# Kernel optimization log

Measured on AMD Instinct MI355X. Metric: run time of the kernel, lower is better.

Reference implementation:

```python
import jax, jax.numpy as jnp
import numpy as np
from jax import lax

PC_RANGE = (-54.0, -54.0, -5.0, 54.0, 54.0, 3.0)
HEIGHTS = (-1.0, 0.0, 1.0)  # all within [z_min, z_max]
IMG_H, IMG_W = 256.0, 704.0  # batch_input_shape of the camera image
BN_EPS = 1e-5


def setup_inputs() -> dict:
    key = jax.random.key(0)
    ks = jax.random.split(key, 11)
    d = {}
    d['radar_bev'] = jax.random.normal(ks[0], (2, 384, 180, 180), jnp.float32)
    d['img_feat'] = jax.random.normal(ks[1], (2, 256, 64, 176), jnp.float32)
    d['lidar2img'] = jax.random.normal(ks[2], (2, 3, 4), jnp.float32)
    d['w1'] = jax.random.normal(ks[3], (384, 256, 1, 1), jnp.float32) * 0.05
    d['bn1'] = jax.random.uniform(ks[4], (4, 384), jnp.float32, 0.1, 1.0)
    d['w2'] = jax.random.normal(ks[5], (384, 384, 3, 3), jnp.float32) * 0.02
    d['bn2'] = jax.random.uniform(ks[6], (4, 384), jnp.float32, 0.1, 1.0)
    d['wf1'] = jax.random.normal(ks[7], (384, 768, 3, 3), jnp.float32) * 0.02
    d['bnf1'] = jax.random.uniform(ks[8], (4, 384), jnp.float32, 0.1, 1.0)
    d['wf2'] = jax.random.normal(ks[9], (384, 384, 3, 3), jnp.float32) * 0.02
    d['bnf2'] = jax.random.uniform(ks[10], (4, 384), jnp.float32, 0.1, 1.0)
    return d


def _conv(x, w, pad):
    return lax.conv_general_dilated(x, w, (1, 1), [(pad, pad), (pad, pad)],
                                    dimension_numbers=('NCHW', 'OIHW', 'NCHW'))


def _bn_relu(x, p):
    g, b, m, v = p[0], p[1], p[2], p[3]
    y = (x - m[:, None, None]) * (g[:, None, None] / jnp.sqrt(v[:, None, None] + BN_EPS)) + b[:, None, None]
    return jax.nn.relu(y)


def _bilinear_sample(img, gx, gy):
    # img: [C,H,W]; gx,gy: [N] normalized coords in grid_sample convention
    # (align_corners=False, padding_mode='zeros')
    C, H, W = img.shape
    ix = ((gx + 1.0) * W - 1.0) * 0.5
    iy = ((gy + 1.0) * H - 1.0) * 0.5
    x0 = jnp.floor(ix); y0 = jnp.floor(iy)
    wx1 = ix - x0; wx0 = 1.0 - wx1
    wy1 = iy - y0; wy0 = 1.0 - wy1

    def corner(xc, yc, w):
        inb = (xc >= 0) & (xc < W) & (yc >= 0) & (yc < H)
        xi = jnp.clip(xc, 0, W - 1).astype(jnp.int32)
        yi = jnp.clip(yc, 0, H - 1).astype(jnp.int32)
        return img[:, yi, xi] * (w * inb)[None, :]

    return (corner(x0, y0, wx0 * wy0) + corner(x0 + 1, y0, wx1 * wy0)
            + corner(x0, y0 + 1, wx0 * wy1) + corner(x0 + 1, y0 + 1, wx1 * wy1))


def reference(radar_bev, img_feat, lidar2img, w1, bn1, w2, bn2, wf1, bnf1, wf2, bnf2):
    B, _, bev_h, bev_w = radar_bev.shape
    x_min, y_min, z_min, x_max, y_max, z_max = PC_RANGE
    xs = jnp.linspace(x_min, x_max, bev_w + 1, dtype=jnp.float32)[:-1] + (x_max - x_min) / bev_w * 0.5
    ys = jnp.linspace(y_min, y_max, bev_h + 1, dtype=jnp.float32)[:-1] + (y_max - y_min) / bev_h * 0.5
    gy, gx = jnp.meshgrid(ys, xs, indexing='ij')  # [bev_h, bev_w]
    zs = jnp.asarray(HEIGHTS, jnp.float32)
    Z = zs.shape[0]
    # points: [Z, bev_h, bev_w, 4] -> [N, 4]
    pts = jnp.stack([jnp.broadcast_to(gx, (Z, bev_h, bev_w)),
                     jnp.broadcast_to(gy, (Z, bev_h, bev_w)),
                     jnp.broadcast_to(zs[:, None, None], (Z, bev_h, bev_w)),
                     jnp.ones((Z, bev_h, bev_w), jnp.float32)], axis=-1).reshape(-1, 4)
    # project: [B, N, 3]
    proj = jnp.einsum('nk,bjk->bnj', pts, lidar2img)
    depth = jnp.maximum(proj[:, :, 2], 1e-5)
    px = proj[:, :, 0] / depth
    py = proj[:, :, 1] / depth
    norm_x = px / IMG_W * 2.0 - 1.0
    norm_y = py / IMG_H * 2.0 - 1.0
    sampled = jax.vmap(_bilinear_sample)(img_feat, norm_x, norm_y)  # [B, C, N]
    valid = ((px >= 0) & (px < IMG_W) & (py >= 0) & (py < IMG_H)
             & (proj[:, :, 2] > 1e-5)).astype(jnp.float32)  # [B, N]
    C = img_feat.shape[1]
    sampled = sampled.reshape(B, C, Z, bev_h, bev_w)
    valid = valid.reshape(B, 1, Z, bev_h, bev_w)
    image_bev = (sampled * valid).sum(axis=2) / jnp.maximum(valid.sum(axis=2), 1.0)
    # image_bev_encoder: 1x1 conv -> BN -> ReLU -> 3x3 conv -> BN -> ReLU
    h = _bn_relu(_conv(image_bev, w1, 0), bn1)
    h = _bn_relu(_conv(h, w2, 1), bn2)
    # bev_fusion on concat(radar, image_bev)
    f = jnp.concatenate([radar_bev, h], axis=1)
    f = _bn_relu(_conv(f, wf1, 1), bnf1)
    f = _bn_relu(_conv(f, wf2, 1), bnf2)
    return f
```

## Files before the change

kernel.cpp:

```cpp
#include <hip/hip_runtime.h>
#include <hip/hip_bf16.h>

#define BEV 180
#define NPOS (BEV * BEV)
#define MTOT (2 * NPOS)
#define IH 64
#define IW 176
#define CIMG 256

typedef __attribute__((ext_vector_type(8))) short bf16x8;
typedef __attribute__((ext_vector_type(4))) float f32x4;

__device__ __forceinline__ void gload_lds16(const void* g, void* l) {
  __builtin_amdgcn_global_load_lds(
      (const __attribute__((address_space(1))) void*)g,
      (__attribute__((address_space(3))) void*)l, 16, 0, 0);
}

__global__ void k_zero(unsigned long long* p) { p[threadIdx.x] = 0ULL; }

template <typename OT>
__device__ __forceinline__ OT conv_out(float v);
template <>
__device__ __forceinline__ float conv_out<float>(float v) { return v; }
template <>
__device__ __forceinline__ __hip_bfloat16 conv_out<__hip_bfloat16>(float v) { return __float2bfloat16(v); }

template <typename OT>
__global__ void k_transpose(const float* __restrict__ in, OT* __restrict__ out, int R, int CL) {
  __shared__ float tile[32][33];
  const float* inb = in + (size_t)blockIdx.z * R * CL;
  OT* outb = out + (size_t)blockIdx.z * R * CL;
  int c0 = blockIdx.x * 32, r0 = blockIdx.y * 32;
  int tx = threadIdx.x, ty = threadIdx.y;
#pragma unroll
  for (int i = 0; i < 32; i += 8) {
    int r = r0 + ty + i, c = c0 + tx;
    tile[ty + i][tx] = (r < R && c < CL) ? inb[(size_t)r * CL + c] : 0.f;
  }
  __syncthreads();
#pragma unroll
  for (int i = 0; i < 32; i += 8) {
    int c = c0 + ty + i, r = r0 + tx;
    if (c < CL && r < R) outb[(size_t)c * R + r] = conv_out<OT>(tile[tx][ty + i]);
  }
}

__global__ void k_sample(const float* __restrict__ imgT, const float* __restrict__ l2i,
                         __hip_bfloat16* __restrict__ out) {
  int blk = blockIdx.x;
  int b = blk / NPOS, rem = blk - b * NPOS;
  int hy = rem / BEV, wx = rem - hy * BEV;
  int c = threadIdx.x;
  float gx = -54.f + 0.3f + 0.6f * (float)wx;
  float gy = -54.f + 0.3f + 0.6f * (float)hy;
  const float* L = l2i + b * 12;
  const float* img = imgT + (size_t)b * (IH * IW * CIMG);
  float acc = 0.f, vcnt = 0.f;
#pragma unroll
  for (int zi = 0; zi < 3; ++zi) {
    float z = (float)(zi - 1);
    float p0 = L[0] * gx + L[1] * gy + L[2] * z + L[3];
    float p1 = L[4] * gx + L[5] * gy + L[6] * z + L[7];
    float p2 = L[8] * gx + L[9] * gy + L[10] * z + L[11];
    float d = fmaxf(p2, 1e-5f);
    float px = p0 / d, py = p1 / d;
    if (px >= 0.f && px < 704.f && py >= 0.f && py < 256.f && p2 > 1e-5f) {
      vcnt += 1.f;
      float ix = px * 0.25f - 0.5f, iy = py * 0.25f - 0.5f;
      float xf = floorf(ix), yf = floorf(iy);
      float wx1 = ix - xf, wy1 = iy - yf;
      float wx0 = 1.f - wx1, wy0 = 1.f - wy1;
      int x0 = (int)xf, y0 = (int)yf;
      int x1 = x0 + 1, y1 = y0 + 1;
      bool bx0 = (unsigned)x0 < IW, bx1 = (unsigned)x1 < IW;
      bool by0 = (unsigned)y0 < IH, by1 = (unsigned)y1 < IH;
      float s = 0.f;
      if (bx0 && by0) s += wx0 * wy0 * img[((size_t)y0 * IW + x0) * CIMG + c];
      if (bx1 && by0) s += wx1 * wy0 * img[((size_t)y0 * IW + x1) * CIMG + c];
      if (bx0 && by1) s += wx0 * wy1 * img[((size_t)y1 * IW + x0) * CIMG + c];
      if (bx1 && by1) s += wx1 * wy1 * img[((size_t)y1 * IW + x1) * CIMG + c];
      acc += s;
    }
  }
  out[(size_t)blk * CIMG + c] = __float2bfloat16(acc / fmaxf(vcnt, 1.f));
}

__global__ void k_packw(const float* __restrict__ w, __hip_bfloat16* __restrict__ wp,
                        int Co, int Ci, int T) {
  size_t idx = (size_t)blockIdx.x * 256 + threadIdx.x;
  size_t tot = (size_t)Co * Ci * T;
  if (idx >= tot) return;
  int ci = (int)(idx % Ci);
  size_t r = idx / Ci;
  int co = (int)(r % Co);
  int tap = (int)(r / Co);
  wp[idx] = __float2bfloat16(w[((size_t)co * Ci + ci) * T + tap]);
}

__global__ void k_packbn(const float* __restrict__ bn, float* __restrict__ sb, int C) {
  int i = blockIdx.x * blockDim.x + threadIdx.x;
  if (i >= C) return;
  float g = bn[i], b = bn[C + i], m = bn[2 * C + i], v = bn[3 * C + i];
  float s = g / sqrtf(v + 1e-5f);
  sb[i] = s;
  sb[C + i] = b - m * s;
}

template <int TAPS>
__global__ __launch_bounds__(256, 2) void k_conv(
    const __hip_bfloat16* __restrict__ x0, const __hip_bfloat16* __restrict__ x1,
    int cin0, int cin1,
    const __hip_bfloat16* __restrict__ wp, const float* __restrict__ sb,
    int isFinal,
    __hip_bfloat16* __restrict__ obf, float* __restrict__ of32,
    const __hip_bfloat16* __restrict__ zp) {
  const int Cout = 384;
  __shared__ __hip_bfloat16 As[384 * 64];
  __shared__ __hip_bfloat16 Bs[2][128 * 64];
  const int t = threadIdx.x;
  const int w = t >> 6, l = t & 63;
  const int bid = blockIdx.x;
  const int b = bid / 120;
  const int rr = bid - b * 120;
  const int y0 = (rr / 12) * 18;
  const int x0c = (rr - (rr / 12) * 12) * 16;
  const int n0 = blockIdx.y * 128;
  const int cinTot = cin0 + cin1;
  const size_t tapStride = (size_t)Cout * cinTot * 2;
  const int nA0 = cin0 >> 6, nA1 = cin1 >> 6, nA = nA0 + nA1;
  const int P = nA * TAPS;

  const int baseRow = t >> 3;
  const int cb = ((t & 7) ^ (baseRow & 7)) * 16;
  int posIdx[12];
  unsigned okMask = 0;
#pragma unroll
  for (int j = 0; j < 12; ++j) {
    int row = j * 32 + baseRow;
    int yy = row / 18, xx = row - yy * 18;
    int ys = y0 - 1 + yy, xg = x0c - 1 + xx;
    if (row < 360 && (unsigned)ys < 180u && (unsigned)xg < 180u) okMask |= (1u << j);
    posIdx[j] = b * NPOS + ys * BEV + xg;
  }
  size_t bOff[4];
#pragma unroll
  for (int j = 0; j < 4; ++j)
    bOff[j] = (size_t)(n0 + j * 32 + baseRow) * (size_t)(cinTot * 2) + (size_t)cb;

  auto issueA = [&](int kc) {
    int s1 = (kc >= nA0);
    int kcw = kc - (s1 ? nA0 : 0);
    const char* xb = s1 ? (const char*)x1 : (const char*)x0;
    size_t cinB = (size_t)(s1 ? cin1 : cin0) * 2;
    size_t ko = (size_t)kcw * 128 + (size_t)cb;
    char* dst = (char*)As + w * 1024;
#pragma unroll
    for (int j = 0; j < 12; ++j) {
      const char* src = ((okMask >> j) & 1) ? (xb + (size_t)posIdx[j] * cinB + ko)
                                            : (const char*)zp;
      gload_lds16(src, dst + j * 4096);
    }
  };
  auto issueB = [&](int q, int kc, int tq) {
    int s1 = (kc >= nA0);
    int kcw = kc - (s1 ? nA0 : 0);
    int segoff = s1 ? cin0 : 0;
    const char* wt = (const char*)wp + (size_t)tq * tapStride + (size_t)(segoff + kcw * 64) * 2;
    char* dst = (char*)Bs[q & 1] + w * 1024;
#pragma unroll
    for (int j = 0; j < 4; ++j) gload_lds16(wt + bOff[j], dst + j * 4096);
  };

  f32x4 acc[9][4];
#pragma unroll
  for (int mi = 0; mi < 9; ++mi)
#pragma unroll
    for (int ni = 0; ni < 4; ++ni) acc[mi][ni] = f32x4{0.f, 0.f, 0.f, 0.f};

  const int wq = w >> 1;
  const int wn = (w & 1) * 64;
  const int xl = l & 15, kq = l >> 4;

  issueA(0);
  issueB(0, 0, 0);

  int kc = 0, tap = 0;
  for (int p = 0; p < P; ++p) {
    if (p + 1 < P) {
      int tq = tap + 1, kn = kc;
      if (tq == TAPS) { tq = 0; ++kn; }
      issueB(p + 1, kn, tq);
      asm volatile("s_waitcnt vmcnt(4)" ::: "memory");
    } else {
      asm volatile("s_waitcnt vmcnt(0)" ::: "memory");
    }
    __builtin_amdgcn_s_barrier();
    asm volatile("" ::: "memory");

    const int dy = (TAPS == 9) ? (tap / 3 - 1) : 0;
    const int dx = (TAPS == 9) ? (tap - (tap / 3) * 3 - 1) : 0;
    const int sRow0 = (wq * 9 + dy + 1) * 18 + xl + dx + 1;
    const char* bLds = (const char*)Bs[p & 1];
    __builtin_amdgcn_s_setprio(1);
#pragma unroll
    for (int ks = 0; ks < 2; ++ks) {
      const int g = ks * 4 + kq;
      bf16x8 af[9], bfr[4];
#pragma unroll
      for (int mi = 0; mi < 9; ++mi) {
        int s = sRow0 + mi * 18;
        af[mi] = *(const bf16x8*)((const char*)As + s * 128 + ((g ^ (s & 7)) * 16));
      }
#pragma unroll
      for (int ni = 0; ni < 4; ++ni) {
        int rB = wn + ni * 16 + xl;
        bfr[ni] = *(const bf16x8*)(bLds + rB * 128 + ((g ^ (rB & 7)) * 16));
      }
#pragma unroll
      for (int mi = 0; mi < 9; ++mi)
#pragma unroll
        for (int ni = 0; ni < 4; ++ni)
          acc[mi][ni] = __builtin_amdgcn_mfma_f32_16x16x32_bf16(af[mi], bfr[ni], acc[mi][ni], 0, 0, 0);
    }
    __builtin_amdgcn_s_setprio(0);
    asm volatile("" ::: "memory");
    __builtin_amdgcn_s_barrier();

    if (tap == TAPS - 1 && kc + 1 < nA) issueA(kc + 1);
    if (++tap == TAPS) { tap = 0; ++kc; }
  }

  float sc[4], bi[4];
#pragma unroll
  for (int ni = 0; ni < 4; ++ni) {
    int cc = n0 + wn + ni * 16 + xl;
    sc[ni] = sb[cc];
    bi[ni] = sb[Cout + cc];
  }
#pragma unroll
  for (int mi = 0; mi < 9; ++mi) {
    int y = y0 + wq * 9 + mi;
#pragma unroll
    for (int j = 0; j < 4; ++j) {
      int x = x0c + kq * 4 + j;
      if (x >= BEV) continue;
      int pp = b * NPOS + y * BEV + x;
#pragma unroll
      for (int ni = 0; ni < 4; ++ni) {
        int cc = n0 + wn + ni * 16 + xl;
        float v = fmaxf(acc[mi][ni][j] * sc[ni] + bi[ni], 0.f);
        if (isFinal) {
          of32[((size_t)(b * Cout + cc)) * NPOS + (size_t)y * BEV + x] = v;
        } else {
          obf[(size_t)pp * Cout + cc] = __float2bfloat16(v);
        }
      }
    }
  }
}

extern "C" void kernel_launch(void* const* d_in, const int* in_sizes, int n_in,
                              void* d_out, int out_size, void* d_ws, size_t ws_size,
                              hipStream_t stream) {
  const float* radar = (const float*)d_in[0];
  const float* imgf = (const float*)d_in[1];
  const float* l2i = (const float*)d_in[2];
  const float* w1 = (const float*)d_in[3];
  const float* bn1 = (const float*)d_in[4];
  const float* w2 = (const float*)d_in[5];
  const float* bn2 = (const float*)d_in[6];
  const float* wf1 = (const float*)d_in[7];
  const float* bnf1 = (const float*)d_in[8];
  const float* wf2 = (const float*)d_in[9];
  const float* bnf2 = (const float*)d_in[10];

  char* ws = (char*)d_ws;
  size_t off = 0;
  auto alloc = [&](size_t bytes) {
    char* p = ws + off;
    off += (bytes + 255) & ~(size_t)255;
    return p;
  };
  char* zp = alloc(4096);
  char* imgT = alloc((size_t)2 * IH * IW * CIMG * 4);
  char* ibev = alloc((size_t)MTOT * CIMG * 2);
  char* radarT = imgT;
  char* h1 = alloc((size_t)MTOT * 384 * 2);
  char* h2 = alloc((size_t)MTOT * 384 * 2);
  char* f1 = h1;
  char* wp1 = alloc((size_t)1 * 384 * 256 * 2);
  char* wp2 = alloc((size_t)9 * 384 * 384 * 2);
  char* wpf1 = alloc((size_t)9 * 384 * 768 * 2);
  char* wpf2 = alloc((size_t)9 * 384 * 384 * 2);
  char* sb1 = alloc(2 * 384 * 4);
  char* sb2 = alloc(2 * 384 * 4);
  char* sbf1 = alloc(2 * 384 * 4);
  char* sbf2 = alloc(2 * 384 * 4);

  k_zero<<<1, 512, 0, stream>>>((unsigned long long*)zp);

  dim3 tb(32, 8);
  k_transpose<float><<<dim3((IH * IW + 31) / 32, (CIMG + 31) / 32, 2), tb, 0, stream>>>(
      imgf, (float*)imgT, CIMG, IH * IW);

  auto packw = [&](const float* src, char* dst, int Co, int Ci, int T) {
    size_t tot = (size_t)Co * Ci * T;
    k_packw<<<(unsigned)((tot + 255) / 256), 256, 0, stream>>>(src, (__hip_bfloat16*)dst, Co, Ci, T);
  };
  packw(w1, wp1, 384, 256, 1);
  packw(w2, wp2, 384, 384, 9);
  packw(wf1, wpf1, 384, 768, 9);
  packw(wf2, wpf2, 384, 384, 9);
  k_packbn<<<2, 256, 0, stream>>>(bn1, (float*)sb1, 384);
  k_packbn<<<2, 256, 0, stream>>>(bn2, (float*)sb2, 384);
  k_packbn<<<2, 256, 0, stream>>>(bnf1, (float*)sbf1, 384);
  k_packbn<<<2, 256, 0, stream>>>(bnf2, (float*)sbf2, 384);

  k_sample<<<MTOT, 256, 0, stream>>>((const float*)imgT, l2i, (__hip_bfloat16*)ibev);

  dim3 cg(240, 3);
  k_conv<1><<<cg, 256, 0, stream>>>((const __hip_bfloat16*)ibev, nullptr, 256, 0,
                                    (const __hip_bfloat16*)wp1, (const float*)sb1, 0,
                                    (__hip_bfloat16*)h1, nullptr, (const __hip_bfloat16*)zp);
  k_transpose<__hip_bfloat16><<<dim3((NPOS + 31) / 32, (384 + 31) / 32, 2), tb, 0, stream>>>(
      radar, (__hip_bfloat16*)radarT, 384, NPOS);
  k_conv<9><<<cg, 256, 0, stream>>>((const __hip_bfloat16*)h1, nullptr, 384, 0,
                                    (const __hip_bfloat16*)wp2, (const float*)sb2, 0,
                                    (__hip_bfloat16*)h2, nullptr, (const __hip_bfloat16*)zp);
  k_conv<9><<<cg, 256, 0, stream>>>((const __hip_bfloat16*)radarT, (const __hip_bfloat16*)h2, 384, 384,
                                    (const __hip_bfloat16*)wpf1, (const float*)sbf1, 0,
                                    (__hip_bfloat16*)f1, nullptr, (const __hip_bfloat16*)zp);
  k_conv<9><<<cg, 256, 0, stream>>>((const __hip_bfloat16*)f1, nullptr, 384, 0,
                                    (const __hip_bfloat16*)wpf2, (const float*)sbf2, 1,
                                    nullptr, (float*)d_out, (const __hip_bfloat16*)zp);
}
```

Measured before the change: 981.2 us.

## Switch conv to 32x32x16 MFMA with 16-row spatial tiles

Replaces the 16x16x32 bf16 MFMA accumulators with 32x32x16 MFMA tiles, each covering two 16-wide image rows against 32 output channels. The spatial tile shrinks from 18 to 16 rows, so the grid grows from 240 to 288 blocks per output-channel group and the LDS halo buffer shrinks. The larger MFMA shape needs fewer LDS fragment loads per FLOP. In exchange, the last tile row block (y 176..191) is partly out of range, which wastes some compute and needs extra store bounds checks.

```diff
diff --git a/kernel.cpp b/kernel.cpp
--- a/kernel.cpp
+++ b/kernel.cpp
@@ -10,6 +10,7 @@
 
 typedef __attribute__((ext_vector_type(8))) short bf16x8;
 typedef __attribute__((ext_vector_type(4))) float f32x4;
+typedef __attribute__((ext_vector_type(16))) float f32x16;
 
 __device__ __forceinline__ void gload_lds16(const void* g, void* l) {
   __builtin_amdgcn_global_load_lds(
@@ -116,14 +117,14 @@
     __hip_bfloat16* __restrict__ obf, float* __restrict__ of32,
     const __hip_bfloat16* __restrict__ zp) {
   const int Cout = 384;
-  __shared__ __hip_bfloat16 As[384 * 64];
+  __shared__ __hip_bfloat16 As[352 * 64];
   __shared__ __hip_bfloat16 Bs[2][128 * 64];
   const int t = threadIdx.x;
   const int w = t >> 6, l = t & 63;
   const int bid = blockIdx.x;
-  const int b = bid / 120;
-  const int rr = bid - b * 120;
-  const int y0 = (rr / 12) * 18;
+  const int b = bid / 144;
+  const int rr = bid - b * 144;
+  const int y0 = (rr / 12) * 16;
   const int x0c = (rr - (rr / 12) * 12) * 16;
   const int n0 = blockIdx.y * 128;
   const int cinTot = cin0 + cin1;
@@ -133,14 +134,14 @@
 
   const int baseRow = t >> 3;
   const int cb = ((t & 7) ^ (baseRow & 7)) * 16;
-  int posIdx[12];
+  int posIdx[11];
   unsigned okMask = 0;
 #pragma unroll
-  for (int j = 0; j < 12; ++j) {
+  for (int j = 0; j < 11; ++j) {
     int row = j * 32 + baseRow;
     int yy = row / 18, xx = row - yy * 18;
     int ys = y0 - 1 + yy, xg = x0c - 1 + xx;
-    if (row < 360 && (unsigned)ys < 180u && (unsigned)xg < 180u) okMask |= (1u << j);
+    if (row < 324 && (unsigned)ys < 180u && (unsigned)xg < 180u) okMask |= (1u << j);
     posIdx[j] = b * NPOS + ys * BEV + xg;
   }
   size_t bOff[4];
@@ -156,7 +157,7 @@
     size_t ko = (size_t)kcw * 128 + (size_t)cb;
     char* dst = (char*)As + w * 1024;
 #pragma unroll
-    for (int j = 0; j < 12; ++j) {
+    for (int j = 0; j < 11; ++j) {
       const char* src = ((okMask >> j) & 1) ? (xb + (size_t)posIdx[j] * cinB + ko)
                                             : (const char*)zp;
       gload_lds16(src, dst + j * 4096);
@@ -172,15 +173,19 @@
     for (int j = 0; j < 4; ++j) gload_lds16(wt + bOff[j], dst + j * 4096);
   };
 
-  f32x4 acc[9][4];
-#pragma unroll
-  for (int mi = 0; mi < 9; ++mi)
-#pragma unroll
-    for (int ni = 0; ni < 4; ++ni) acc[mi][ni] = f32x4{0.f, 0.f, 0.f, 0.f};
+  f32x16 acc[4][2];
+#pragma unroll
+  for (int mf = 0; mf < 4; ++mf)
+#pragma unroll
+    for (int nf = 0; nf < 2; ++nf)
+#pragma unroll
+      for (int j = 0; j < 16; ++j) acc[mf][nf][j] = 0.f;
 
   const int wq = w >> 1;
   const int wn = (w & 1) * 64;
-  const int xl = l & 15, kq = l >> 4;
+  const int xl = l & 15;
+  const int yh = (l >> 4) & 1;
+  const int kh = l >> 5;
 
   issueA(0);
   issueB(0, 0, 0);
@@ -200,28 +205,29 @@
 
     const int dy = (TAPS == 9) ? (tap / 3 - 1) : 0;
     const int dx = (TAPS == 9) ? (tap - (tap / 3) * 3 - 1) : 0;
-    const int sRow0 = (wq * 9 + dy + 1) * 18 + xl + dx + 1;
+    const int sRow0 = (wq * 8 + yh + dy + 1) * 18 + xl + dx + 1;
     const char* bLds = (const char*)Bs[p & 1];
+    const int rB0 = wn + (l & 31);
     __builtin_amdgcn_s_setprio(1);
 #pragma unroll
-    for (int ks = 0; ks < 2; ++ks) {
-      const int g = ks * 4 + kq;
-      bf16x8 af[9], bfr[4];
-#pragma unroll
-      for (int mi = 0; mi < 9; ++mi) {
-        int s = sRow0 + mi * 18;
-        af[mi] = *(const bf16x8*)((const char*)As + s * 128 + ((g ^ (s & 7)) * 16));
+    for (int kst = 0; kst < 4; ++kst) {
+      const int c16 = kst * 2 + kh;
+      bf16x8 af[4], bfr[2];
+#pragma unroll
+      for (int mf = 0; mf < 4; ++mf) {
+        int s = sRow0 + mf * 2 * 18;
+        af[mf] = *(const bf16x8*)((const char*)As + s * 128 + ((c16 ^ (s & 7)) * 16));
       }
 #pragma unroll
-      for (int ni = 0; ni < 4; ++ni) {
-        int rB = wn + ni * 16 + xl;
-        bfr[ni] = *(const bf16x8*)(bLds + rB * 128 + ((g ^ (rB & 7)) * 16));
+      for (int nf = 0; nf < 2; ++nf) {
+        int rB = rB0 + nf * 32;
+        bfr[nf] = *(const bf16x8*)(bLds + rB * 128 + ((c16 ^ (rB & 7)) * 16));
       }
 #pragma unroll
-      for (int mi = 0; mi < 9; ++mi)
-#pragma unroll
-        for (int ni = 0; ni < 4; ++ni)
-          acc[mi][ni] = __builtin_amdgcn_mfma_f32_16x16x32_bf16(af[mi], bfr[ni], acc[mi][ni], 0, 0, 0);
+      for (int mf = 0; mf < 4; ++mf)
+#pragma unroll
+        for (int nf = 0; nf < 2; ++nf)
+          acc[mf][nf] = __builtin_amdgcn_mfma_f32_32x32x16_bf16(af[mf], bfr[nf], acc[mf][nf], 0, 0, 0);
     }
     __builtin_amdgcn_s_setprio(0);
     asm volatile("" ::: "memory");
@@ -231,25 +237,26 @@
     if (++tap == TAPS) { tap = 0; ++kc; }
   }
 
-  float sc[4], bi[4];
-#pragma unroll
-  for (int ni = 0; ni < 4; ++ni) {
-    int cc = n0 + wn + ni * 16 + xl;
-    sc[ni] = sb[cc];
-    bi[ni] = sb[Cout + cc];
-  }
-#pragma unroll
-  for (int mi = 0; mi < 9; ++mi) {
-    int y = y0 + wq * 9 + mi;
-#pragma unroll
-    for (int j = 0; j < 4; ++j) {
-      int x = x0c + kq * 4 + j;
-      if (x >= BEV) continue;
+  float sc[2], bi[2];
+#pragma unroll
+  for (int nf = 0; nf < 2; ++nf) {
+    int cc = n0 + wn + nf * 32 + (l & 31);
+    sc[nf] = sb[cc];
+    bi[nf] = sb[Cout + cc];
+  }
+#pragma unroll
+  for (int mf = 0; mf < 4; ++mf) {
+#pragma unroll
+    for (int j = 0; j < 16; ++j) {
+      int r = (j & 3) + 8 * (j >> 2) + 4 * kh;
+      int y = y0 + wq * 8 + mf * 2 + (r >> 4);
+      int x = x0c + (r & 15);
+      if (y >= BEV || x >= BEV) continue;
       int pp = b * NPOS + y * BEV + x;
 #pragma unroll
-      for (int ni = 0; ni < 4; ++ni) {
-        int cc = n0 + wn + ni * 16 + xl;
-        float v = fmaxf(acc[mi][ni][j] * sc[ni] + bi[ni], 0.f);
+      for (int nf = 0; nf < 2; ++nf) {
+        int cc = n0 + wn + nf * 32 + (l & 31);
+        float v = fmaxf(acc[mf][nf][j] * sc[nf] + bi[nf], 0.f);
         if (isFinal) {
           of32[((size_t)(b * Cout + cc)) * NPOS + (size_t)y * BEV + x] = v;
         } else {
@@ -319,7 +326,7 @@
 
   k_sample<<<MTOT, 256, 0, stream>>>((const float*)imgT, l2i, (__hip_bfloat16*)ibev);
 
-  dim3 cg(240, 3);
+  dim3 cg(288, 3);
   k_conv<1><<<cg, 256, 0, stream>>>((const __hip_bfloat16*)ibev, nullptr, 256, 0,
                                     (const __hip_bfloat16*)wp1, (const float*)sb1, 0,
                                     (__hip_bfloat16*)h1, nullptr, (const __hip_bfloat16*)zp);
```

Measured after the change: 1.007 ms. 1.03x slower.
